# Optimization experiments

Measured on AMD Instinct MI355X. Metric: run time of the kernel, lower is better.

## Reference

```python
import jax, jax.numpy as jnp
import numpy as np

N_NODES = 50000
EPS = 1e-12  # F.normalize eps


def _gcn_layer(x, W, b, src, dst):
    # GCNConv(normalize=False): h = x @ W, then sum-aggregate messages from
    # source nodes into target nodes along edge_index, then add bias.
    h = x @ W
    agg = jax.ops.segment_sum(h[src], dst, num_segments=N_NODES)
    out = agg + b
    # F.normalize(p=2, dim=-1) then ReLU
    norm = jnp.linalg.norm(out, axis=-1, keepdims=True)
    out = out / jnp.maximum(norm, EPS)
    return jax.nn.relu(out)


def setup_inputs() -> dict:
    key = jax.random.key(0)
    ks = jax.random.split(key, 8)
    nfeat, nhid, nclass, n_edges = 128, 128, 40, 640000
    x = jax.random.normal(ks[0], (N_NODES, nfeat), dtype=jnp.float32)
    edge_index = jax.random.randint(ks[1], (2, n_edges), 0, N_NODES, dtype=jnp.int64)
    s = 1.0 / np.sqrt(nhid)
    return {
        "x": x,
        "edge_index": edge_index,
        "W1": jax.random.normal(ks[2], (nfeat, nhid), jnp.float32) * s,
        "b1": jnp.zeros((nhid,), jnp.float32),
        "W2": jax.random.normal(ks[3], (nhid, nhid), jnp.float32) * s,
        "b2": jnp.zeros((nhid,), jnp.float32),
        "W3": jax.random.normal(ks[4], (nhid, nhid), jnp.float32) * s,
        "b3": jnp.zeros((nhid,), jnp.float32),
        "W4": jax.random.normal(ks[5], (nhid, nhid), jnp.float32) * s,
        "b4": jnp.zeros((nhid,), jnp.float32),
        "Wl": jax.random.normal(ks[6], (nhid, nclass), jnp.float32) * s,
        "bl": jnp.zeros((nclass,), jnp.float32),
    }


def reference(x, edge_index, W1, b1, W2, b2, W3, b3, W4, b4, Wl, bl):
    src, dst = edge_index[0], edge_index[1]
    x1 = _gcn_layer(x, W1, b1, src, dst)
    x2 = _gcn_layer(x1, W2, b2, src, dst)
    x3 = _gcn_layer(x2, W3, b3, src, dst)
    x4 = _gcn_layer(x3, W4, b4, src, dst)
    logits = x4 @ Wl + bl
    probs = jax.nn.softmax(logits, axis=-1)
    return (logits, probs, x4)
```

## Files before the change

kernel.cpp:

```cpp
#include <hip/hip_runtime.h>
#include <hip/hip_bf16.h>
#include <hip/hip_fp16.h>
#include <math.h>

#define NFEAT 128
#define NCLASS 40

typedef __attribute__((ext_vector_type(8))) short frag_ab;
typedef __attribute__((ext_vector_type(4))) float frag_cd;

static __device__ inline unsigned short f2bf_rne(float f) {
    union { float f; unsigned u; } v;
    v.f = f;
    unsigned r = v.u + 0x7FFFu + ((v.u >> 16) & 1u);
    return (unsigned short)(r >> 16);
}
static __device__ inline float bf2f(unsigned short h) {
    union { unsigned u; float f; } v;
    v.u = ((unsigned)h) << 16;
    return v.f;
}


__global__ __launch_bounds__(256) void hist_kernel(const int* __restrict__ dst,
                                                   int* __restrict__ counts, int n_edges) {
    int i = blockIdx.x * 256 + threadIdx.x;
    int n4 = n_edges >> 2;
    if (i < n4) {
        int4 d = ((const int4*)dst)[i];
        atomicAdd(&counts[d.x], 1);
        atomicAdd(&counts[d.y], 1);
        atomicAdd(&counts[d.z], 1);
        atomicAdd(&counts[d.w], 1);
    }
    if (i == 0) {
        for (int e = n4 << 2; e < n_edges; ++e) atomicAdd(&counts[dst[e]], 1);
    }
}

__global__ __launch_bounds__(256) void scan1_kernel(const int* __restrict__ cnt,
                                                    int* __restrict__ excl,
                                                    int* __restrict__ bsums, int n) {
    __shared__ int sd[256];
    int t = threadIdx.x;
    int i = blockIdx.x * 256 + t;
    int v = (i < n) ? cnt[i] : 0;
    sd[t] = v;
    __syncthreads();
#pragma unroll
    for (int off = 1; off < 256; off <<= 1) {
        int tmp = (t >= off) ? sd[t - off] : 0;
        __syncthreads();
        sd[t] += tmp;
        __syncthreads();
    }
    if (i < n) excl[i] = sd[t] - v;
    if (t == 255) bsums[blockIdx.x] = sd[255];
}

__global__ __launch_bounds__(256) void scan2_kernel(int* __restrict__ bsums, int nb) {
    __shared__ int sd[256];
    int t = threadIdx.x;
    int v = (t < nb) ? bsums[t] : 0;
    sd[t] = v;
    __syncthreads();
#pragma unroll
    for (int off = 1; off < 256; off <<= 1) {
        int tmp = (t >= off) ? sd[t - off] : 0;
        __syncthreads();
        sd[t] += tmp;
        __syncthreads();
    }
    if (t < nb) bsums[t] = sd[t] - v;
    if (t == 255) bsums[nb] = sd[255];
}

__global__ __launch_bounds__(256) void scan3_kernel(const int* __restrict__ excl,
                                                    const int* __restrict__ bsums,
                                                    int* __restrict__ row_ptr,
                                                    int* __restrict__ woff, int n, int nb) {
    int i = blockIdx.x * 256 + threadIdx.x;
    if (i < n) {
        int v = excl[i] + bsums[blockIdx.x];
        row_ptr[i] = v;
        woff[i] = v;
    }
    if (i == 0) row_ptr[n] = bsums[nb];
}

__global__ __launch_bounds__(256) void scatter_kernel(const int* __restrict__ src,
                                                      const int* __restrict__ dst,
                                                      int* __restrict__ woff,
                                                      int* __restrict__ src_sorted, int n_edges) {
    int i = blockIdx.x * 256 + threadIdx.x;
    int n4 = n_edges >> 2;
    if (i < n4) {
        int4 d = ((const int4*)dst)[i];
        int4 s = ((const int4*)src)[i];
        int p0 = atomicAdd(&woff[d.x], 1);
        int p1 = atomicAdd(&woff[d.y], 1);
        int p2 = atomicAdd(&woff[d.z], 1);
        int p3 = atomicAdd(&woff[d.w], 1);
        src_sorted[p0] = s.x;
        src_sorted[p1] = s.y;
        src_sorted[p2] = s.z;
        src_sorted[p3] = s.w;
    }
    if (i == 0) {
        for (int e = n4 << 2; e < n_edges; ++e) {
            int p = atomicAdd(&woff[dst[e]], 1);
            src_sorted[p] = src[e];
        }
    }
}


__global__ __launch_bounds__(256) void conv_h_kernel(const float* __restrict__ in,
                                                     __half* __restrict__ out, int n4) {
    int i = blockIdx.x * 256 + threadIdx.x;
    if (i < n4) {
        float4 v = ((const float4*)in)[i];
        __half2 h0 = __floats2half2_rn(v.x, v.y);
        __half2 h1 = __floats2half2_rn(v.z, v.w);
        ((__half2*)out)[i * 2 + 0] = h0;
        ((__half2*)out)[i * 2 + 1] = h1;
    }
}


__global__ __launch_bounds__(256) void agg_h_kernel(const __half* __restrict__ xin,
                                                    const int* __restrict__ row_ptr,
                                                    const int* __restrict__ src_sorted,
                                                    float* __restrict__ agg, int n_nodes) {
    int node = blockIdx.x * 16 + (threadIdx.x >> 4);
    if (node >= n_nodes) return;
    int c = threadIdx.x & 15;
    int jb = row_ptr[node], je = row_ptr[node + 1];
    const uint4* xp = (const uint4*)xin;

    float a[8];
#pragma unroll
    for (int i = 0; i < 8; ++i) a[i] = 0.f;

    int j = jb;
    for (; j + 3 < je; j += 4) {
        int s0 = src_sorted[j];
        int s1 = src_sorted[j + 1];
        int s2 = src_sorted[j + 2];
        int s3 = src_sorted[j + 3];
        uint4 r0 = xp[s0 * 16 + c];
        uint4 r1 = xp[s1 * 16 + c];
        uint4 r2 = xp[s2 * 16 + c];
        uint4 r3 = xp[s3 * 16 + c];
#pragma unroll
        for (int q = 0; q < 4; ++q) {
            unsigned u0 = (&r0.x)[q], u1 = (&r1.x)[q], u2 = (&r2.x)[q], u3 = (&r3.x)[q];
            float2 f0 = __half22float2(*(__half2*)&u0);
            float2 f1 = __half22float2(*(__half2*)&u1);
            float2 f2 = __half22float2(*(__half2*)&u2);
            float2 f3 = __half22float2(*(__half2*)&u3);
            a[q * 2 + 0] += f0.x + f1.x + f2.x + f3.x;
            a[q * 2 + 1] += f0.y + f1.y + f2.y + f3.y;
        }
    }
    for (; j < je; ++j) {
        int s0 = src_sorted[j];
        uint4 r0 = xp[s0 * 16 + c];
#pragma unroll
        for (int q = 0; q < 4; ++q) {
            unsigned u0 = (&r0.x)[q];
            float2 f0 = __half22float2(*(__half2*)&u0);
            a[q * 2 + 0] += f0.x;
            a[q * 2 + 1] += f0.y;
        }
    }
    float4* op = (float4*)agg + (size_t)node * 32 + c * 2;
    op[0] = make_float4(a[0], a[1], a[2], a[3]);
    op[1] = make_float4(a[4], a[5], a[6], a[7]);
}


__global__ __launch_bounds__(256) void wprep_kernel(const float* __restrict__ W0,
                                                    const float* __restrict__ W1,
                                                    const float* __restrict__ W2,
                                                    const float* __restrict__ W3,
                                                    short* __restrict__ whi,
                                                    short* __restrict__ wlo) {
    int layer = blockIdx.y;
    const float* W = layer == 0 ? W0 : layer == 1 ? W1 : layer == 2 ? W2 : W3;
    short* h = whi + (size_t)layer * 16384;
    short* l = wlo + (size_t)layer * 16384;
    int idx = blockIdx.x * 256 + threadIdx.x;
    int lane = idx & 63;
    int t = (idx >> 6) & 7;
    int s = idx >> 9;
    int quad = lane >> 4;
    int n = lane & 15;
    int kbase = s * 32 + quad * 8;
    int col = t * 16 + n;
#pragma unroll
    for (int j = 0; j < 8; ++j) {
        float f = W[(size_t)(kbase + j) * NFEAT + col];
        unsigned short hb = f2bf_rne(f);
        unsigned short lb = f2bf_rne(f - bf2f(hb));
        h[(size_t)idx * 8 + j] = (short)hb;
        l[(size_t)idx * 8 + j] = (short)lb;
    }
}


__global__ __launch_bounds__(256) void gemm_mfma_kernel(const float* __restrict__ A,
                                                        const short* __restrict__ whi,
                                                        const short* __restrict__ wlo,
                                                        const float* __restrict__ bias,
                                                        float* __restrict__ outf,
                                                        __half* __restrict__ outh, int M) {
    int tid = threadIdx.x;
    int wave = tid >> 6;
    int lane = tid & 63;
    int quad = lane >> 4;
    int n16 = lane & 15;
    int base = blockIdx.x * 64;

    int arow = base + wave * 16 + n16;
    int arc = arow < M ? arow : M - 1;
    const float* Ar = A + (size_t)arc * NFEAT;

    const frag_ab* WH = (const frag_ab*)whi;
    const frag_ab* WL = (const frag_ab*)wlo;

    frag_cd acc[8];
#pragma unroll
    for (int t = 0; t < 8; ++t) acc[t] = (frag_cd){0.f, 0.f, 0.f, 0.f};

#pragma unroll
    for (int s = 0; s < 4; ++s) {
        const float* ap = Ar + s * 32 + quad * 8;
        float4 x0 = *(const float4*)ap;
        float4 x1 = *(const float4*)(ap + 4);
        float xs[8] = {x0.x, x0.y, x0.z, x0.w, x1.x, x1.y, x1.z, x1.w};
        frag_ab ah, al;
#pragma unroll
        for (int j = 0; j < 8; ++j) {
            unsigned short hb = f2bf_rne(xs[j]);
            ah[j] = (short)hb;
            al[j] = (short)f2bf_rne(xs[j] - bf2f(hb));
        }
#pragma unroll
        for (int t = 0; t < 8; ++t) {
            frag_ab bh = WH[(s * 8 + t) * 64 + lane];
            frag_ab bl = WL[(s * 8 + t) * 64 + lane];
            acc[t] = __builtin_amdgcn_mfma_f32_16x16x32_bf16(ah, bh, acc[t], 0, 0, 0);
            acc[t] = __builtin_amdgcn_mfma_f32_16x16x32_bf16(ah, bl, acc[t], 0, 0, 0);
            acc[t] = __builtin_amdgcn_mfma_f32_16x16x32_bf16(al, bh, acc[t], 0, 0, 0);
        }
    }

    float ssq[4] = {0.f, 0.f, 0.f, 0.f};
#pragma unroll
    for (int t = 0; t < 8; ++t) {
        float bv = bias[t * 16 + n16];
#pragma unroll
        for (int r = 0; r < 4; ++r) {
            acc[t][r] += bv;
            ssq[r] += acc[t][r] * acc[t][r];
        }
    }
#pragma unroll
    for (int mask = 1; mask <= 8; mask <<= 1) {
#pragma unroll
        for (int r = 0; r < 4; ++r) ssq[r] += __shfl_xor(ssq[r], mask);
    }
    float inv[4];
#pragma unroll
    for (int r = 0; r < 4; ++r) inv[r] = 1.0f / fmaxf(sqrtf(ssq[r]), 1e-12f);

    int orow0 = base + wave * 16 + quad * 4;
#pragma unroll
    for (int r = 0; r < 4; ++r) {
        int orow = orow0 + r;
        if (orow < M) {
            if (outh) {
                __half* op = outh + (size_t)orow * NFEAT + n16;
#pragma unroll
                for (int t = 0; t < 8; ++t)
                    op[t * 16] = __float2half(fmaxf(acc[t][r] * inv[r], 0.f));
            } else {
                float* op = outf + (size_t)orow * NFEAT + n16;
#pragma unroll
                for (int t = 0; t < 8; ++t)
                    op[t * 16] = fmaxf(acc[t][r] * inv[r], 0.f);
            }
        }
    }
}


__global__ __launch_bounds__(256) void classifier_kernel(const float* __restrict__ x4,
                                                         const float* __restrict__ Wl,
                                                         const float* __restrict__ bl,
                                                         float* __restrict__ logits,
                                                         float* __restrict__ probs, int n_nodes) {
    int node = blockIdx.x * 256 + threadIdx.x;
    int nc = node < n_nodes ? node : n_nodes - 1;
    const float* row = x4 + (size_t)nc * NFEAT;

    float acc[NCLASS];
#pragma unroll
    for (int c = 0; c < NCLASS; ++c) acc[c] = bl[c];

    for (int k = 0; k < NFEAT; k += 4) {
        float4 a = *(const float4*)(row + k);
#pragma unroll
        for (int kk = 0; kk < 4; ++kk) {
            float av = (&a.x)[kk];
            const float* Wr = Wl + (k + kk) * NCLASS;
#pragma unroll
            for (int c = 0; c < NCLASS; ++c) acc[c] += av * Wr[c];
        }
    }

    float m = acc[0];
#pragma unroll
    for (int c = 1; c < NCLASS; ++c) m = fmaxf(m, acc[c]);
    float ex[NCLASS];
    float sum = 0.f;
#pragma unroll
    for (int c = 0; c < NCLASS; ++c) {
        ex[c] = __expf(acc[c] - m);
        sum += ex[c];
    }
    float is = 1.0f / sum;

    if (node < n_nodes) {
        float4* lo = (float4*)(logits + (size_t)node * NCLASS);
        float4* po = (float4*)(probs + (size_t)node * NCLASS);
#pragma unroll
        for (int c = 0; c < NCLASS; c += 4) {
            float4 lv, pv;
            lv.x = acc[c + 0]; lv.y = acc[c + 1]; lv.z = acc[c + 2]; lv.w = acc[c + 3];
            pv.x = ex[c + 0] * is; pv.y = ex[c + 1] * is; pv.z = ex[c + 2] * is; pv.w = ex[c + 3] * is;
            lo[c >> 2] = lv;
            po[c >> 2] = pv;
        }
    }
}


extern "C" void kernel_launch(void* const* d_in, const int* in_sizes, int n_in,
                              void* d_out, int out_size, void* d_ws, size_t ws_size,
                              hipStream_t stream) {
    const float* x  = (const float*)d_in[0];
    const int*   ei = (const int*)d_in[1];
    const float* W1 = (const float*)d_in[2];
    const float* b1 = (const float*)d_in[3];
    const float* W2 = (const float*)d_in[4];
    const float* b2 = (const float*)d_in[5];
    const float* W3 = (const float*)d_in[6];
    const float* b3 = (const float*)d_in[7];
    const float* W4 = (const float*)d_in[8];
    const float* b4 = (const float*)d_in[9];
    const float* Wl = (const float*)d_in[10];
    const float* bl = (const float*)d_in[11];

    const int n_nodes = in_sizes[0] / NFEAT;
    const int n_edges = in_sizes[1] / 2;
    const int* src = ei;
    const int* dst = ei + n_edges;

    float* out    = (float*)d_out;
    float* logits = out;
    float* probs  = out + (size_t)n_nodes * NCLASS;
    float* x4     = out + 2 * (size_t)n_nodes * NCLASS;

    char* ws = (char*)d_ws;
    size_t off = 0;
    auto wsalloc = [&](size_t bytes) -> void* {
        void* p = ws + off;
        off += (bytes + 255) & ~(size_t)255;
        return p;
    };
    float*  agg        = (float*)wsalloc((size_t)n_nodes * NFEAT * sizeof(float));
    __half* xh         = (__half*)wsalloc((size_t)n_nodes * NFEAT * sizeof(__half));
    int*    row_ptr    = (int*)wsalloc(((size_t)n_nodes + 1) * sizeof(int));
    int*    woff       = (int*)wsalloc((size_t)n_nodes * sizeof(int));
    int*    cnt        = (int*)wsalloc((size_t)n_nodes * sizeof(int));
    int*    src_sorted = (int*)wsalloc((size_t)n_edges * sizeof(int));
    int     nb         = (n_nodes + 255) / 256;
    int*    bsums      = (int*)wsalloc(((size_t)nb + 1) * sizeof(int));
    short*  whi        = (short*)wsalloc((size_t)4 * 16384 * sizeof(short));
    short*  wlo        = (short*)wsalloc((size_t)4 * 16384 * sizeof(short));

    hipMemsetAsync(cnt, 0, (size_t)n_nodes * sizeof(int), stream);

    wprep_kernel<<<dim3(8, 4), 256, 0, stream>>>(W1, W2, W3, W4, whi, wlo);

    int xc4 = (n_nodes * NFEAT) / 4;
    conv_h_kernel<<<(xc4 + 255) / 256, 256, 0, stream>>>(x, xh, xc4);

    int e4b = ((n_edges >> 2) + 255) / 256;
    hist_kernel<<<e4b, 256, 0, stream>>>(dst, cnt, n_edges);
    scan1_kernel<<<nb, 256, 0, stream>>>(cnt, row_ptr , bsums, n_nodes);
    scan2_kernel<<<1, 256, 0, stream>>>(bsums, nb);
    scan3_kernel<<<nb, 256, 0, stream>>>(row_ptr, bsums, row_ptr, woff, n_nodes, nb);
    scatter_kernel<<<e4b, 256, 0, stream>>>(src, dst, woff, src_sorted, n_edges);

    int ah = (n_nodes + 15) / 16;
    int gb = (n_nodes + 63) / 64;
    int cb = (n_nodes + 255) / 256;

    agg_h_kernel<<<ah, 256, 0, stream>>>(xh, row_ptr, src_sorted, agg, n_nodes);
    gemm_mfma_kernel<<<gb, 256, 0, stream>>>(agg, whi + 0 * 16384, wlo + 0 * 16384, b1, nullptr, xh, n_nodes);
    agg_h_kernel<<<ah, 256, 0, stream>>>(xh, row_ptr, src_sorted, agg, n_nodes);
    gemm_mfma_kernel<<<gb, 256, 0, stream>>>(agg, whi + 1 * 16384, wlo + 1 * 16384, b2, nullptr, xh, n_nodes);
    agg_h_kernel<<<ah, 256, 0, stream>>>(xh, row_ptr, src_sorted, agg, n_nodes);
    gemm_mfma_kernel<<<gb, 256, 0, stream>>>(agg, whi + 2 * 16384, wlo + 2 * 16384, b3, nullptr, xh, n_nodes);
    agg_h_kernel<<<ah, 256, 0, stream>>>(xh, row_ptr, src_sorted, agg, n_nodes);
    gemm_mfma_kernel<<<gb, 256, 0, stream>>>(agg, whi + 3 * 16384, wlo + 3 * 16384, b4, x4, nullptr, n_nodes);

    classifier_kernel<<<cb, 256, 0, stream>>>(x4, Wl, bl, logits, probs, n_nodes);
}
```

Measured before the change: 380.8 us.

## Fuse CSR build, layers and classifier into one cooperative persistent kernel

Replaces the chain of about fifteen separate kernel launches (histogram, three-pass scan, scatter, four aggregate+GEMM pairs, classifier) with one cooperative persistent kernel that uses grid-wide syncs between phases. The three small prep kernels (fp16 conversion, count zeroing, weight splitting) are merged into a single launch that also replaces the memset. The aim is to remove launch overhead and inter-kernel gaps. In exchange the grid is capped at occupancy×256 blocks, at most 1024, so each phase runs grid-stride loops with less parallelism, and every grid.sync has its own cost.

```diff
diff --git a/kernel.cpp b/kernel.cpp
--- a/kernel.cpp
+++ b/kernel.cpp
@@ -1,10 +1,14 @@
 #include <hip/hip_runtime.h>
 #include <hip/hip_bf16.h>
 #include <hip/hip_fp16.h>
+#include <hip/hip_cooperative_groups.h>
 #include <math.h>
+
+namespace cg = cooperative_groups;
 
 #define NFEAT 128
 #define NCLASS 40
+#define NCU 256
 
 typedef __attribute__((ext_vector_type(8))) short frag_ab;
 typedef __attribute__((ext_vector_type(4))) float frag_cd;
@@ -22,327 +26,335 @@
 }
 
 
-__global__ __launch_bounds__(256) void hist_kernel(const int* __restrict__ dst,
-                                                   int* __restrict__ counts, int n_edges) {
-    int i = blockIdx.x * 256 + threadIdx.x;
-    int n4 = n_edges >> 2;
-    if (i < n4) {
-        int4 d = ((const int4*)dst)[i];
-        atomicAdd(&counts[d.x], 1);
-        atomicAdd(&counts[d.y], 1);
-        atomicAdd(&counts[d.z], 1);
-        atomicAdd(&counts[d.w], 1);
-    }
-    if (i == 0) {
-        for (int e = n4 << 2; e < n_edges; ++e) atomicAdd(&counts[dst[e]], 1);
+__global__ __launch_bounds__(256) void prep_kernel(const float* __restrict__ x,
+                                                   __half* __restrict__ xh, int xc4,
+                                                   int* __restrict__ cnt, int n_nodes,
+                                                   const float* __restrict__ W0,
+                                                   const float* __restrict__ W1,
+                                                   const float* __restrict__ W2,
+                                                   const float* __restrict__ W3,
+                                                   short* __restrict__ whi,
+                                                   short* __restrict__ wlo,
+                                                   int convB, int zeroB) {
+    int b = blockIdx.x;
+    if (b < convB) {
+        int i = b * 256 + threadIdx.x;
+        if (i < xc4) {
+            float4 v = ((const float4*)x)[i];
+            ((__half2*)xh)[i * 2 + 0] = __floats2half2_rn(v.x, v.y);
+            ((__half2*)xh)[i * 2 + 1] = __floats2half2_rn(v.z, v.w);
+        }
+    } else if (b < convB + zeroB) {
+        int i = (b - convB) * 256 + threadIdx.x;
+        if (i < n_nodes) cnt[i] = 0;
+    } else {
+        int wb = b - convB - zeroB;
+        int layer = wb >> 3;
+        const float* W = layer == 0 ? W0 : layer == 1 ? W1 : layer == 2 ? W2 : W3;
+        short* h = whi + (size_t)layer * 16384;
+        short* l = wlo + (size_t)layer * 16384;
+        int idx = (wb & 7) * 256 + threadIdx.x;
+        int lane = idx & 63;
+        int t = (idx >> 6) & 7;
+        int s = idx >> 9;
+        int quad = lane >> 4;
+        int n = lane & 15;
+        int kbase = s * 32 + quad * 8;
+        int col = t * 16 + n;
+#pragma unroll
+        for (int j = 0; j < 8; ++j) {
+            float f = W[(size_t)(kbase + j) * NFEAT + col];
+            unsigned short hb = f2bf_rne(f);
+            unsigned short lb = f2bf_rne(f - bf2f(hb));
+            h[(size_t)idx * 8 + j] = (short)hb;
+            l[(size_t)idx * 8 + j] = (short)lb;
+        }
     }
 }
 
-__global__ __launch_bounds__(256) void scan1_kernel(const int* __restrict__ cnt,
-                                                    int* __restrict__ excl,
-                                                    int* __restrict__ bsums, int n) {
+
+struct MegaP {
+    const int* src;
+    const int* dst;
+    int n_edges;
+    int n_nodes;
+    int nbt;
+    int* cnt;
+    int* row_ptr;
+    int* woff;
+    int* bsums;
+    int* src_sorted;
+    __half* xh;
+    float* agg;
+    const short* whi;
+    const short* wlo;
+    const float* b1; const float* b2; const float* b3; const float* b4;
+    float* x4;
+    const float* Wl;
+    const float* bl;
+    float* logits;
+    float* probs;
+};
+
+__global__ __launch_bounds__(256, 4) void mega_kernel(MegaP p) {
+    cg::grid_group grid = cg::this_grid();
     __shared__ int sd[256];
-    int t = threadIdx.x;
-    int i = blockIdx.x * 256 + t;
-    int v = (i < n) ? cnt[i] : 0;
-    sd[t] = v;
-    __syncthreads();
-#pragma unroll
-    for (int off = 1; off < 256; off <<= 1) {
-        int tmp = (t >= off) ? sd[t - off] : 0;
+    const int tid = threadIdx.x;
+    const int gid = blockIdx.x * 256 + tid;
+    const int gsz = gridDim.x * 256;
+    const int n = p.n_nodes;
+
+    {
+        int n4 = p.n_edges >> 2;
+        for (int i = gid; i < n4; i += gsz) {
+            int4 d = ((const int4*)p.dst)[i];
+            atomicAdd(&p.cnt[d.x], 1);
+            atomicAdd(&p.cnt[d.y], 1);
+            atomicAdd(&p.cnt[d.z], 1);
+            atomicAdd(&p.cnt[d.w], 1);
+        }
+        if (gid == 0) {
+            for (int e = n4 << 2; e < p.n_edges; ++e) atomicAdd(&p.cnt[p.dst[e]], 1);
+        }
+    }
+    grid.sync();
+
+    for (int t = blockIdx.x; t < p.nbt; t += gridDim.x) {
+        int i = t * 256 + tid;
+        int v = (i < n) ? p.cnt[i] : 0;
+        sd[tid] = v;
         __syncthreads();
-        sd[t] += tmp;
+#pragma unroll
+        for (int off = 1; off < 256; off <<= 1) {
+            int tmp = (tid >= off) ? sd[tid - off] : 0;
+            __syncthreads();
+            sd[tid] += tmp;
+            __syncthreads();
+        }
+        if (i < n) p.row_ptr[i] = sd[tid] - v;
+        if (tid == 255) p.bsums[t] = sd[255];
         __syncthreads();
     }
-    if (i < n) excl[i] = sd[t] - v;
-    if (t == 255) bsums[blockIdx.x] = sd[255];
-}
-
-__global__ __launch_bounds__(256) void scan2_kernel(int* __restrict__ bsums, int nb) {
-    __shared__ int sd[256];
-    int t = threadIdx.x;
-    int v = (t < nb) ? bsums[t] : 0;
-    sd[t] = v;
-    __syncthreads();
-#pragma unroll
-    for (int off = 1; off < 256; off <<= 1) {
-        int tmp = (t >= off) ? sd[t - off] : 0;
+    grid.sync();
+
+    if (blockIdx.x == 0) {
+        int v = (tid < p.nbt) ? p.bsums[tid] : 0;
+        sd[tid] = v;
         __syncthreads();
-        sd[t] += tmp;
-        __syncthreads();
-    }
-    if (t < nb) bsums[t] = sd[t] - v;
-    if (t == 255) bsums[nb] = sd[255];
-}
-
-__global__ __launch_bounds__(256) void scan3_kernel(const int* __restrict__ excl,
-                                                    const int* __restrict__ bsums,
-                                                    int* __restrict__ row_ptr,
-                                                    int* __restrict__ woff, int n, int nb) {
-    int i = blockIdx.x * 256 + threadIdx.x;
-    if (i < n) {
-        int v = excl[i] + bsums[blockIdx.x];
-        row_ptr[i] = v;
-        woff[i] = v;
-    }
-    if (i == 0) row_ptr[n] = bsums[nb];
-}
-
-__global__ __launch_bounds__(256) void scatter_kernel(const int* __restrict__ src,
-                                                      const int* __restrict__ dst,
-                                                      int* __restrict__ woff,
-                                                      int* __restrict__ src_sorted, int n_edges) {
-    int i = blockIdx.x * 256 + threadIdx.x;
-    int n4 = n_edges >> 2;
-    if (i < n4) {
-        int4 d = ((const int4*)dst)[i];
-        int4 s = ((const int4*)src)[i];
-        int p0 = atomicAdd(&woff[d.x], 1);
-        int p1 = atomicAdd(&woff[d.y], 1);
-        int p2 = atomicAdd(&woff[d.z], 1);
-        int p3 = atomicAdd(&woff[d.w], 1);
-        src_sorted[p0] = s.x;
-        src_sorted[p1] = s.y;
-        src_sorted[p2] = s.z;
-        src_sorted[p3] = s.w;
-    }
-    if (i == 0) {
-        for (int e = n4 << 2; e < n_edges; ++e) {
-            int p = atomicAdd(&woff[dst[e]], 1);
-            src_sorted[p] = src[e];
-        }
-    }
-}
-
-
-__global__ __launch_bounds__(256) void conv_h_kernel(const float* __restrict__ in,
-                                                     __half* __restrict__ out, int n4) {
-    int i = blockIdx.x * 256 + threadIdx.x;
-    if (i < n4) {
-        float4 v = ((const float4*)in)[i];
-        __half2 h0 = __floats2half2_rn(v.x, v.y);
-        __half2 h1 = __floats2half2_rn(v.z, v.w);
-        ((__half2*)out)[i * 2 + 0] = h0;
-        ((__half2*)out)[i * 2 + 1] = h1;
-    }
-}
-
-
-__global__ __launch_bounds__(256) void agg_h_kernel(const __half* __restrict__ xin,
-                                                    const int* __restrict__ row_ptr,
-                                                    const int* __restrict__ src_sorted,
-                                                    float* __restrict__ agg, int n_nodes) {
-    int node = blockIdx.x * 16 + (threadIdx.x >> 4);
-    if (node >= n_nodes) return;
-    int c = threadIdx.x & 15;
-    int jb = row_ptr[node], je = row_ptr[node + 1];
-    const uint4* xp = (const uint4*)xin;
-
-    float a[8];
-#pragma unroll
-    for (int i = 0; i < 8; ++i) a[i] = 0.f;
-
-    int j = jb;
-    for (; j + 3 < je; j += 4) {
-        int s0 = src_sorted[j];
-        int s1 = src_sorted[j + 1];
-        int s2 = src_sorted[j + 2];
-        int s3 = src_sorted[j + 3];
-        uint4 r0 = xp[s0 * 16 + c];
-        uint4 r1 = xp[s1 * 16 + c];
-        uint4 r2 = xp[s2 * 16 + c];
-        uint4 r3 = xp[s3 * 16 + c];
-#pragma unroll
-        for (int q = 0; q < 4; ++q) {
-            unsigned u0 = (&r0.x)[q], u1 = (&r1.x)[q], u2 = (&r2.x)[q], u3 = (&r3.x)[q];
-            float2 f0 = __half22float2(*(__half2*)&u0);
-            float2 f1 = __half22float2(*(__half2*)&u1);
-            float2 f2 = __half22float2(*(__half2*)&u2);
-            float2 f3 = __half22float2(*(__half2*)&u3);
-            a[q * 2 + 0] += f0.x + f1.x + f2.x + f3.x;
-            a[q * 2 + 1] += f0.y + f1.y + f2.y + f3.y;
-        }
-    }
-    for (; j < je; ++j) {
-        int s0 = src_sorted[j];
-        uint4 r0 = xp[s0 * 16 + c];
-#pragma unroll
-        for (int q = 0; q < 4; ++q) {
-            unsigned u0 = (&r0.x)[q];
-            float2 f0 = __half22float2(*(__half2*)&u0);
-            a[q * 2 + 0] += f0.x;
-            a[q * 2 + 1] += f0.y;
-        }
-    }
-    float4* op = (float4*)agg + (size_t)node * 32 + c * 2;
-    op[0] = make_float4(a[0], a[1], a[2], a[3]);
-    op[1] = make_float4(a[4], a[5], a[6], a[7]);
-}
-
-
-__global__ __launch_bounds__(256) void wprep_kernel(const float* __restrict__ W0,
-                                                    const float* __restrict__ W1,
-                                                    const float* __restrict__ W2,
-                                                    const float* __restrict__ W3,
-                                                    short* __restrict__ whi,
-                                                    short* __restrict__ wlo) {
-    int layer = blockIdx.y;
-    const float* W = layer == 0 ? W0 : layer == 1 ? W1 : layer == 2 ? W2 : W3;
-    short* h = whi + (size_t)layer * 16384;
-    short* l = wlo + (size_t)layer * 16384;
-    int idx = blockIdx.x * 256 + threadIdx.x;
-    int lane = idx & 63;
-    int t = (idx >> 6) & 7;
-    int s = idx >> 9;
-    int quad = lane >> 4;
-    int n = lane & 15;
-    int kbase = s * 32 + quad * 8;
-    int col = t * 16 + n;
-#pragma unroll
-    for (int j = 0; j < 8; ++j) {
-        float f = W[(size_t)(kbase + j) * NFEAT + col];
-        unsigned short hb = f2bf_rne(f);
-        unsigned short lb = f2bf_rne(f - bf2f(hb));
-        h[(size_t)idx * 8 + j] = (short)hb;
-        l[(size_t)idx * 8 + j] = (short)lb;
-    }
-}
-
-
-__global__ __launch_bounds__(256) void gemm_mfma_kernel(const float* __restrict__ A,
-                                                        const short* __restrict__ whi,
-                                                        const short* __restrict__ wlo,
-                                                        const float* __restrict__ bias,
-                                                        float* __restrict__ outf,
-                                                        __half* __restrict__ outh, int M) {
-    int tid = threadIdx.x;
-    int wave = tid >> 6;
-    int lane = tid & 63;
-    int quad = lane >> 4;
-    int n16 = lane & 15;
-    int base = blockIdx.x * 64;
-
-    int arow = base + wave * 16 + n16;
-    int arc = arow < M ? arow : M - 1;
-    const float* Ar = A + (size_t)arc * NFEAT;
-
-    const frag_ab* WH = (const frag_ab*)whi;
-    const frag_ab* WL = (const frag_ab*)wlo;
-
-    frag_cd acc[8];
-#pragma unroll
-    for (int t = 0; t < 8; ++t) acc[t] = (frag_cd){0.f, 0.f, 0.f, 0.f};
-
-#pragma unroll
-    for (int s = 0; s < 4; ++s) {
-        const float* ap = Ar + s * 32 + quad * 8;
-        float4 x0 = *(const float4*)ap;
-        float4 x1 = *(const float4*)(ap + 4);
-        float xs[8] = {x0.x, x0.y, x0.z, x0.w, x1.x, x1.y, x1.z, x1.w};
-        frag_ab ah, al;
-#pragma unroll
-        for (int j = 0; j < 8; ++j) {
-            unsigned short hb = f2bf_rne(xs[j]);
-            ah[j] = (short)hb;
-            al[j] = (short)f2bf_rne(xs[j] - bf2f(hb));
-        }
-#pragma unroll
-        for (int t = 0; t < 8; ++t) {
-            frag_ab bh = WH[(s * 8 + t) * 64 + lane];
-            frag_ab bl = WL[(s * 8 + t) * 64 + lane];
-            acc[t] = __builtin_amdgcn_mfma_f32_16x16x32_bf16(ah, bh, acc[t], 0, 0, 0);
-            acc[t] = __builtin_amdgcn_mfma_f32_16x16x32_bf16(ah, bl, acc[t], 0, 0, 0);
-            acc[t] = __builtin_amdgcn_mfma_f32_16x16x32_bf16(al, bh, acc[t], 0, 0, 0);
-        }
-    }
-
-    float ssq[4] = {0.f, 0.f, 0.f, 0.f};
-#pragma unroll
-    for (int t = 0; t < 8; ++t) {
-        float bv = bias[t * 16 + n16];
-#pragma unroll
-        for (int r = 0; r < 4; ++r) {
-            acc[t][r] += bv;
-            ssq[r] += acc[t][r] * acc[t][r];
-        }
-    }
-#pragma unroll
-    for (int mask = 1; mask <= 8; mask <<= 1) {
-#pragma unroll
-        for (int r = 0; r < 4; ++r) ssq[r] += __shfl_xor(ssq[r], mask);
-    }
-    float inv[4];
-#pragma unroll
-    for (int r = 0; r < 4; ++r) inv[r] = 1.0f / fmaxf(sqrtf(ssq[r]), 1e-12f);
-
-    int orow0 = base + wave * 16 + quad * 4;
-#pragma unroll
-    for (int r = 0; r < 4; ++r) {
-        int orow = orow0 + r;
-        if (orow < M) {
-            if (outh) {
-                __half* op = outh + (size_t)orow * NFEAT + n16;
-#pragma unroll
-                for (int t = 0; t < 8; ++t)
-                    op[t * 16] = __float2half(fmaxf(acc[t][r] * inv[r], 0.f));
-            } else {
-                float* op = outf + (size_t)orow * NFEAT + n16;
-#pragma unroll
-                for (int t = 0; t < 8; ++t)
-                    op[t * 16] = fmaxf(acc[t][r] * inv[r], 0.f);
+#pragma unroll
+        for (int off = 1; off < 256; off <<= 1) {
+            int tmp = (tid >= off) ? sd[tid - off] : 0;
+            __syncthreads();
+            sd[tid] += tmp;
+            __syncthreads();
+        }
+        if (tid < p.nbt) p.bsums[tid] = sd[tid] - v;
+        if (tid == 255) p.bsums[p.nbt] = sd[255];
+    }
+    grid.sync();
+
+    for (int t = blockIdx.x; t < p.nbt; t += gridDim.x) {
+        int i = t * 256 + tid;
+        if (i < n) {
+            int v = p.row_ptr[i] + p.bsums[t];
+            p.row_ptr[i] = v;
+            p.woff[i] = v;
+        }
+    }
+    if (gid == 0) p.row_ptr[n] = p.bsums[p.nbt];
+    grid.sync();
+
+    {
+        int n4 = p.n_edges >> 2;
+        for (int i = gid; i < n4; i += gsz) {
+            int4 d = ((const int4*)p.dst)[i];
+            int4 s = ((const int4*)p.src)[i];
+            int p0 = atomicAdd(&p.woff[d.x], 1);
+            int p1 = atomicAdd(&p.woff[d.y], 1);
+            int p2 = atomicAdd(&p.woff[d.z], 1);
+            int p3 = atomicAdd(&p.woff[d.w], 1);
+            p.src_sorted[p0] = s.x;
+            p.src_sorted[p1] = s.y;
+            p.src_sorted[p2] = s.z;
+            p.src_sorted[p3] = s.w;
+        }
+        if (gid == 0) {
+            for (int e = n4 << 2; e < p.n_edges; ++e) {
+                int q = atomicAdd(&p.woff[p.dst[e]], 1);
+                p.src_sorted[q] = p.src[e];
             }
         }
     }
-}
-
-
-__global__ __launch_bounds__(256) void classifier_kernel(const float* __restrict__ x4,
-                                                         const float* __restrict__ Wl,
-                                                         const float* __restrict__ bl,
-                                                         float* __restrict__ logits,
-                                                         float* __restrict__ probs, int n_nodes) {
-    int node = blockIdx.x * 256 + threadIdx.x;
-    int nc = node < n_nodes ? node : n_nodes - 1;
-    const float* row = x4 + (size_t)nc * NFEAT;
-
-    float acc[NCLASS];
-#pragma unroll
-    for (int c = 0; c < NCLASS; ++c) acc[c] = bl[c];
-
-    for (int k = 0; k < NFEAT; k += 4) {
-        float4 a = *(const float4*)(row + k);
-#pragma unroll
-        for (int kk = 0; kk < 4; ++kk) {
-            float av = (&a.x)[kk];
-            const float* Wr = Wl + (k + kk) * NCLASS;
-#pragma unroll
-            for (int c = 0; c < NCLASS; ++c) acc[c] += av * Wr[c];
-        }
-    }
-
-    float m = acc[0];
-#pragma unroll
-    for (int c = 1; c < NCLASS; ++c) m = fmaxf(m, acc[c]);
-    float ex[NCLASS];
-    float sum = 0.f;
-#pragma unroll
-    for (int c = 0; c < NCLASS; ++c) {
-        ex[c] = __expf(acc[c] - m);
-        sum += ex[c];
-    }
-    float is = 1.0f / sum;
-
-    if (node < n_nodes) {
-        float4* lo = (float4*)(logits + (size_t)node * NCLASS);
-        float4* po = (float4*)(probs + (size_t)node * NCLASS);
-#pragma unroll
-        for (int c = 0; c < NCLASS; c += 4) {
-            float4 lv, pv;
-            lv.x = acc[c + 0]; lv.y = acc[c + 1]; lv.z = acc[c + 2]; lv.w = acc[c + 3];
-            pv.x = ex[c + 0] * is; pv.y = ex[c + 1] * is; pv.z = ex[c + 2] * is; pv.w = ex[c + 3] * is;
-            lo[c >> 2] = lv;
-            po[c >> 2] = pv;
-        }
+    grid.sync();
+
+    const int NTa = (n + 15) >> 4;
+    const int NTg = (n + 63) >> 6;
+    for (int l = 0; l < 4; ++l) {
+        for (int tg = blockIdx.x; tg < NTa; tg += gridDim.x) {
+            int node = tg * 16 + (tid >> 4);
+            if (node < n) {
+                int c = tid & 15;
+                int jb = p.row_ptr[node], je = p.row_ptr[node + 1];
+                const uint4* xp = (const uint4*)p.xh;
+                float a[8];
+#pragma unroll
+                for (int i = 0; i < 8; ++i) a[i] = 0.f;
+                int j = jb;
+                for (; j + 3 < je; j += 4) {
+                    int s0 = p.src_sorted[j];
+                    int s1 = p.src_sorted[j + 1];
+                    int s2 = p.src_sorted[j + 2];
+                    int s3 = p.src_sorted[j + 3];
+                    uint4 r0 = xp[s0 * 16 + c];
+                    uint4 r1 = xp[s1 * 16 + c];
+                    uint4 r2 = xp[s2 * 16 + c];
+                    uint4 r3 = xp[s3 * 16 + c];
+#pragma unroll
+                    for (int q = 0; q < 4; ++q) {
+                        unsigned u0 = (&r0.x)[q], u1 = (&r1.x)[q], u2 = (&r2.x)[q], u3 = (&r3.x)[q];
+                        float2 f0 = __half22float2(*(__half2*)&u0);
+                        float2 f1 = __half22float2(*(__half2*)&u1);
+                        float2 f2 = __half22float2(*(__half2*)&u2);
+                        float2 f3 = __half22float2(*(__half2*)&u3);
+                        a[q * 2 + 0] += f0.x + f1.x + f2.x + f3.x;
+                        a[q * 2 + 1] += f0.y + f1.y + f2.y + f3.y;
+                    }
+                }
+                for (; j < je; ++j) {
+                    int s0 = p.src_sorted[j];
+                    uint4 r0 = xp[s0 * 16 + c];
+#pragma unroll
+                    for (int q = 0; q < 4; ++q) {
+                        unsigned u0 = (&r0.x)[q];
+                        float2 f0 = __half22float2(*(__half2*)&u0);
+                        a[q * 2 + 0] += f0.x;
+                        a[q * 2 + 1] += f0.y;
+                    }
+                }
+                float4* op = (float4*)p.agg + (size_t)node * 32 + c * 2;
+                op[0] = make_float4(a[0], a[1], a[2], a[3]);
+                op[1] = make_float4(a[4], a[5], a[6], a[7]);
+            }
+        }
+        grid.sync();
+
+        {
+            const float* bias = l == 0 ? p.b1 : l == 1 ? p.b2 : l == 2 ? p.b3 : p.b4;
+            const frag_ab* WH = (const frag_ab*)(p.whi + (size_t)l * 16384);
+            const frag_ab* WL = (const frag_ab*)(p.wlo + (size_t)l * 16384);
+            int wave = tid >> 6;
+            int lane = tid & 63;
+            int quad = lane >> 4;
+            int n16 = lane & 15;
+            for (int tg = blockIdx.x; tg < NTg; tg += gridDim.x) {
+                int base = tg * 64;
+                int arow = base + wave * 16 + n16;
+                int arc = arow < n ? arow : n - 1;
+                const float* Ar = p.agg + (size_t)arc * NFEAT;
+
+                frag_cd acc[8];
+#pragma unroll
+                for (int t = 0; t < 8; ++t) acc[t] = (frag_cd){0.f, 0.f, 0.f, 0.f};
+
+#pragma unroll
+                for (int s = 0; s < 4; ++s) {
+                    const float* ap = Ar + s * 32 + quad * 8;
+                    float4 x0 = *(const float4*)ap;
+                    float4 x1 = *(const float4*)(ap + 4);
+                    float xs[8] = {x0.x, x0.y, x0.z, x0.w, x1.x, x1.y, x1.z, x1.w};
+                    frag_ab ah, al;
+#pragma unroll
+                    for (int j = 0; j < 8; ++j) {
+                        unsigned short hb = f2bf_rne(xs[j]);
+                        ah[j] = (short)hb;
+                        al[j] = (short)f2bf_rne(xs[j] - bf2f(hb));
+                    }
+#pragma unroll
+                    for (int t = 0; t < 8; ++t) {
+                        frag_ab bh = WH[(s * 8 + t) * 64 + lane];
+                        frag_ab bl = WL[(s * 8 + t) * 64 + lane];
+                        acc[t] = __builtin_amdgcn_mfma_f32_16x16x32_bf16(ah, bh, acc[t], 0, 0, 0);
+                        acc[t] = __builtin_amdgcn_mfma_f32_16x16x32_bf16(ah, bl, acc[t], 0, 0, 0);
+                        acc[t] = __builtin_amdgcn_mfma_f32_16x16x32_bf16(al, bh, acc[t], 0, 0, 0);
+                    }
+                }
+
+                float ssq[4] = {0.f, 0.f, 0.f, 0.f};
+#pragma unroll
+                for (int t = 0; t < 8; ++t) {
+                    float bv = bias[t * 16 + n16];
+#pragma unroll
+                    for (int r = 0; r < 4; ++r) {
+                        acc[t][r] += bv;
+                        ssq[r] += acc[t][r] * acc[t][r];
+                    }
+                }
+#pragma unroll
+                for (int mask = 1; mask <= 8; mask <<= 1) {
+#pragma unroll
+                    for (int r = 0; r < 4; ++r) ssq[r] += __shfl_xor(ssq[r], mask);
+                }
+                float inv[4];
+#pragma unroll
+                for (int r = 0; r < 4; ++r) inv[r] = 1.0f / fmaxf(sqrtf(ssq[r]), 1e-12f);
+
+                int orow0 = base + wave * 16 + quad * 4;
+#pragma unroll
+                for (int r = 0; r < 4; ++r) {
+                    int orow = orow0 + r;
+                    if (orow < n) {
+                        if (l < 3) {
+                            __half* op = p.xh + (size_t)orow * NFEAT + n16;
+#pragma unroll
+                            for (int t = 0; t < 8; ++t)
+                                op[t * 16] = __float2half(fmaxf(acc[t][r] * inv[r], 0.f));
+                        } else {
+                            float* op = p.x4 + (size_t)orow * NFEAT + n16;
+#pragma unroll
+                            for (int t = 0; t < 8; ++t)
+                                op[t * 16] = fmaxf(acc[t][r] * inv[r], 0.f);
+                        }
+                    }
+                }
+            }
+        }
+        grid.sync();
+    }
+
+    for (int node = gid; node < n; node += gsz) {
+        const float* row = p.x4 + (size_t)node * NFEAT;
+        float acc[NCLASS];
+#pragma unroll
+        for (int c = 0; c < NCLASS; ++c) acc[c] = p.bl[c];
+        for (int k = 0; k < NFEAT; k += 4) {
+            float4 a = *(const float4*)(row + k);
+#pragma unroll
+            for (int kk = 0; kk < 4; ++kk) {
+                float av = (&a.x)[kk];
+                const float* Wr = p.Wl + (k + kk) * NCLASS;
+#pragma unroll
+                for (int c = 0; c < NCLASS; ++c) acc[c] += av * Wr[c];
+            }
+        }
+        float4* lo = (float4*)(p.logits + (size_t)node * NCLASS);
+#pragma unroll
+        for (int c = 0; c < NCLASS; c += 4)
+            lo[c >> 2] = make_float4(acc[c], acc[c + 1], acc[c + 2], acc[c + 3]);
+
+        float m = acc[0];
+#pragma unroll
+        for (int c = 1; c < NCLASS; ++c) m = fmaxf(m, acc[c]);
+        float sum = 0.f;
+#pragma unroll
+        for (int c = 0; c < NCLASS; ++c) {
+            acc[c] = __expf(acc[c] - m);
+            sum += acc[c];
+        }
+        float is = 1.0f / sum;
+        float4* po = (float4*)(p.probs + (size_t)node * NCLASS);
+#pragma unroll
+        for (int c = 0; c < NCLASS; c += 4)
+            po[c >> 2] = make_float4(acc[c] * is, acc[c + 1] * is, acc[c + 2] * is, acc[c + 3] * is);
     }
 }
 
@@ -386,37 +398,32 @@
     int*    woff       = (int*)wsalloc((size_t)n_nodes * sizeof(int));
     int*    cnt        = (int*)wsalloc((size_t)n_nodes * sizeof(int));
     int*    src_sorted = (int*)wsalloc((size_t)n_edges * sizeof(int));
-    int     nb         = (n_nodes + 255) / 256;
-    int*    bsums      = (int*)wsalloc(((size_t)nb + 1) * sizeof(int));
+    int     nbt        = (n_nodes + 255) / 256;
+    int*    bsums      = (int*)wsalloc(((size_t)nbt + 1) * sizeof(int));
     short*  whi        = (short*)wsalloc((size_t)4 * 16384 * sizeof(short));
     short*  wlo        = (short*)wsalloc((size_t)4 * 16384 * sizeof(short));
 
-    hipMemsetAsync(cnt, 0, (size_t)n_nodes * sizeof(int), stream);
-
-    wprep_kernel<<<dim3(8, 4), 256, 0, stream>>>(W1, W2, W3, W4, whi, wlo);
-
-    int xc4 = (n_nodes * NFEAT) / 4;
-    conv_h_kernel<<<(xc4 + 255) / 256, 256, 0, stream>>>(x, xh, xc4);
-
-    int e4b = ((n_edges >> 2) + 255) / 256;
-    hist_kernel<<<e4b, 256, 0, stream>>>(dst, cnt, n_edges);
-    scan1_kernel<<<nb, 256, 0, stream>>>(cnt, row_ptr , bsums, n_nodes);
-    scan2_kernel<<<1, 256, 0, stream>>>(bsums, nb);
-    scan3_kernel<<<nb, 256, 0, stream>>>(row_ptr, bsums, row_ptr, woff, n_nodes, nb);
-    scatter_kernel<<<e4b, 256, 0, stream>>>(src, dst, woff, src_sorted, n_edges);
-
-    int ah = (n_nodes + 15) / 16;
-    int gb = (n_nodes + 63) / 64;
-    int cb = (n_nodes + 255) / 256;
-
-    agg_h_kernel<<<ah, 256, 0, stream>>>(xh, row_ptr, src_sorted, agg, n_nodes);
-    gemm_mfma_kernel<<<gb, 256, 0, stream>>>(agg, whi + 0 * 16384, wlo + 0 * 16384, b1, nullptr, xh, n_nodes);
-    agg_h_kernel<<<ah, 256, 0, stream>>>(xh, row_ptr, src_sorted, agg, n_nodes);
-    gemm_mfma_kernel<<<gb, 256, 0, stream>>>(agg, whi + 1 * 16384, wlo + 1 * 16384, b2, nullptr, xh, n_nodes);
-    agg_h_kernel<<<ah, 256, 0, stream>>>(xh, row_ptr, src_sorted, agg, n_nodes);
-    gemm_mfma_kernel<<<gb, 256, 0, stream>>>(agg, whi + 2 * 16384, wlo + 2 * 16384, b3, nullptr, xh, n_nodes);
-    agg_h_kernel<<<ah, 256, 0, stream>>>(xh, row_ptr, src_sorted, agg, n_nodes);
-    gemm_mfma_kernel<<<gb, 256, 0, stream>>>(agg, whi + 3 * 16384, wlo + 3 * 16384, b4, x4, nullptr, n_nodes);
-
-    classifier_kernel<<<cb, 256, 0, stream>>>(x4, Wl, bl, logits, probs, n_nodes);
+    int xc4   = (n_nodes * NFEAT) / 4;
+    int convB = (xc4 + 255) / 256;
+    int zeroB = (n_nodes + 255) / 256;
+    prep_kernel<<<convB + zeroB + 32, 256, 0, stream>>>(x, xh, xc4, cnt, n_nodes,
+                                                        W1, W2, W3, W4, whi, wlo,
+                                                        convB, zeroB);
+
+    MegaP p;
+    p.src = src; p.dst = dst; p.n_edges = n_edges; p.n_nodes = n_nodes; p.nbt = nbt;
+    p.cnt = cnt; p.row_ptr = row_ptr; p.woff = woff; p.bsums = bsums;
+    p.src_sorted = src_sorted; p.xh = xh; p.agg = agg;
+    p.whi = whi; p.wlo = wlo;
+    p.b1 = b1; p.b2 = b2; p.b3 = b3; p.b4 = b4;
+    p.x4 = x4; p.Wl = Wl; p.bl = bl; p.logits = logits; p.probs = probs;
+
+    int maxPerCU = 0;
+    hipOccupancyMaxActiveBlocksPerMultiprocessor(&maxPerCU, mega_kernel, 256, 0);
+    if (maxPerCU < 1) maxPerCU = 1;
+    int grid = maxPerCU * NCU;
+    if (grid > 1024) grid = 1024;
+    void* kargs[] = { (void*)&p };
+    hipLaunchCooperativeKernel((const void*)mega_kernel, dim3(grid), dim3(256),
+                               kargs, 0, stream);
 }
```

Measured after the change: 1.385 ms. 3.64x slower.
